# Kernel optimization log

Measured on AMD Instinct MI355X. Metric: run time of the kernel, lower is better.

Reference implementation:

```python
import jax, jax.numpy as jnp
import numpy as np

B, U1, U2 = 2, 3072, 3072
IF = 256      # in_feat_dim
FD = 256      # feat_dim
M = 4         # num_modes
D = IF // M   # attention_mode_dim = 64
STD = 0.02    # base_initializer_range
LN_EPS = 1e-12


def setup_inputs() -> dict:
    key = jax.random.key(0)
    ks = jax.random.split(key, 8)
    inp = {
        'query_feat': jax.random.normal(ks[0], (B, U1, IF), jnp.float32),
        'key_feat':   jax.random.normal(ks[1], (B, U2, IF), jnp.float32),
        # tied QK projection (key weight == query weight after tie_qk)
        'Wq':    jax.random.normal(ks[2], (M * D, IF), jnp.float32) * STD,
        # value projection of ExpandedFeatTrans.first_linear (v_has_bias=True)
        'Wv':    jax.random.normal(ks[3], (M * FD, IF), jnp.float32) * STD,
        'bv':    jnp.zeros((M * FD,), jnp.float32),
        # MMSharedMid shared linear
        'W_mid': jax.random.normal(ks[4], (FD, FD), jnp.float32) * STD,
        'b_mid': jnp.zeros((FD,), jnp.float32),
        # MMSharedOutput shared linear + LayerNorm
        'W_out': jax.random.normal(ks[5], (FD, FD), jnp.float32) * STD,
        'b_out': jnp.zeros((FD,), jnp.float32),
        'ln_g':  jnp.ones((FD,), jnp.float32),
        'ln_b':  jnp.zeros((FD,), jnp.float32),
        # LearnedSoftAggregate feat2score linear (FD -> 1)
        'W_agg': jax.random.normal(ks[6], (1, FD), jnp.float32) * STD,
        'b_agg': jnp.zeros((1,), jnp.float32),
    }
    return inp


def _layer_norm(x, g, b):
    mu = x.mean(-1, keepdims=True)
    var = ((x - mu) ** 2).mean(-1, keepdims=True)
    return (x - mu) * jax.lax.rsqrt(var + LN_EPS) * g + b


def reference(query_feat, key_feat, Wq, Wv, bv, W_mid, b_mid, W_out, b_out,
              ln_g, ln_b, W_agg, b_agg):
    # --- multi-mode cross attention with tied QK ---
    q = (query_feat @ Wq.T).reshape(B, U1, M, D).transpose(0, 2, 1, 3)  # b m u d
    k = (key_feat   @ Wq.T).reshape(B, U2, M, D).transpose(0, 2, 1, 3)  # b m v d
    scores = jnp.einsum('bmud,bmvd->bmuv', q, k) / np.float32(np.sqrt(D))
    probs = jax.nn.softmax(scores, axis=-1)                              # b m u v

    # --- ExpandedFeatTrans: per-mode value projection + fusion ---
    v = (key_feat @ Wv.T + bv).reshape(B, U2, M, FD).transpose(0, 2, 1, 3)  # b m v f
    fused = jnp.einsum('bmuv,bmvf->bmuf', probs, v)                          # b m u f

    # --- MMSharedMid FFN (shared linear + exact gelu; dropout=0) ---
    mid = jax.nn.gelu(fused @ W_mid.T + b_mid, approximate=False)

    # --- MMSharedOutput: shared linear + residual + LayerNorm ---
    outp = _layer_norm(mid @ W_out.T + b_out + fused, ln_g, ln_b)            # b m u f

    # --- LearnedSoftAggregate over modes (group_dim=1) ---
    mode_scores = (outp @ W_agg.T + b_agg)[..., 0]                           # b m u
    agg_probs = jax.nn.softmax(mode_scores, axis=1)
    trans_feat = (outp * agg_probs[..., None]).sum(axis=1)                   # b u f
    return trans_feat
```

## Files before the change

kernel.cpp:

```cpp
#include <hip/hip_runtime.h>
#include <hip/hip_bf16.h>
#include <cstdint>
#include <cstddef>

typedef __attribute__((ext_vector_type(8))) short     bf16x8;
typedef __attribute__((ext_vector_type(4))) float     f32x4;
typedef __attribute__((ext_vector_type(4))) unsigned short u16x4;

using as1_void = __attribute__((address_space(1))) void;
using as3_void = __attribute__((address_space(3))) void;

#define MFMA16(a,b,c) __builtin_amdgcn_mfma_f32_16x16x32_bf16((a),(b),(c),0,0,0)

__device__ __forceinline__ unsigned short f2bf(float f) {
  union { float f; unsigned u; } v; v.f = f;
  unsigned r = v.u + 0x7fffu + ((v.u >> 16) & 1u);
  return (unsigned short)(r >> 16);
}
__device__ __forceinline__ float bf2f(unsigned short h) {
  union { unsigned u; float f; } v; v.u = ((unsigned)h) << 16; return v.f;
}
__device__ __forceinline__ unsigned cvt_pk_bf16(float lo, float hi) {
  unsigned r;
  asm volatile("v_cvt_pk_bf16_f32 %0, %1, %2" : "=v"(r) : "v"(lo), "v"(hi));
  return r;
}

__device__ __forceinline__ void gload16(const void* g, void* l) {
  __builtin_amdgcn_global_load_lds((const as1_void*)g, (as3_void*)l, 16, 0, 0);
}

constexpr size_t oXq  = 0;
constexpr size_t oXk  = oXq + 1572864ull * 2;
constexpr size_t oWq  = oXk + 1572864ull * 2;
constexpr size_t oWv  = oWq + 65536ull   * 2;
constexpr size_t oWm  = oWv + 262144ull  * 2;
constexpr size_t oWo  = oWm + 65536ull   * 2;
constexpr size_t oQb  = oWo + 65536ull   * 2;
constexpr size_t oKb  = oQb + 1572864ull * 2;
constexpr size_t oVb  = oKb + 1572864ull * 2;
constexpr size_t oPa  = oVb + 6291456ull * 2;
constexpr size_t oMl  = oPa + 12582912ull * 2;

__global__ __launch_bounds__(256) void cvt_kernel(
    const float* __restrict__ q, const float* __restrict__ k,
    const float* __restrict__ wq, const float* __restrict__ wv,
    const float* __restrict__ wm, const float* __restrict__ wo,
    unsigned short* __restrict__ ws) {
  int i4 = (blockIdx.x * 256 + threadIdx.x) * 4;
  const float* src; int local;
  if (i4 < 1572864)       { src = q;  local = i4; }
  else if (i4 < 3145728)  { src = k;  local = i4 - 1572864; }
  else if (i4 < 3211264)  { src = wq; local = i4 - 3145728; }
  else if (i4 < 3473408)  { src = wv; local = i4 - 3211264; }
  else if (i4 < 3538944)  { src = wm; local = i4 - 3473408; }
  else                    { src = wo; local = i4 - 3538944; }
  f32x4 v = *(const f32x4*)(src + local);
  u16x4 o;
  o.x = f2bf(v.x); o.y = f2bf(v.y); o.z = f2bf(v.z); o.w = f2bf(v.w);
  *(u16x4*)(ws + i4) = o;
}

__global__ __launch_bounds__(256) void proj_kernel(const float* __restrict__ bv,
                                                   char* __restrict__ wsb) {
  int lane = threadIdx.x & 63, wid = threadIdx.x >> 6;
  int rowblk = blockIdx.x % 384;
  int ny = blockIdx.x / 384;
  int r0 = rowblk * 16;

  const unsigned short* X = (const unsigned short*)(wsb + (ny == 0 ? oXq : oXk));
  const unsigned short* W;
  if (ny <= 1) W = (const unsigned short*)(wsb + oWq);
  else         W = (const unsigned short*)(wsb + oWv) + (size_t)(ny - 2) * 256 * 256;

  int arow = r0 + (lane & 15);
  const unsigned short* Xp = X + (size_t)arow * 256 + ((lane >> 4) * 8);
  int n0 = wid * 64;

  f32x4 acc[4];
#pragma unroll
  for (int bt = 0; bt < 4; ++bt) acc[bt] = (f32x4){0.f, 0.f, 0.f, 0.f};

#pragma unroll
  for (int ks = 0; ks < 8; ++ks) {
    bf16x8 af = *(const bf16x8*)(Xp + ks * 32);
#pragma unroll
    for (int bt = 0; bt < 4; ++bt) {
      int n = n0 + bt * 16 + (lane & 15);
      bf16x8 bf = *(const bf16x8*)(W + (size_t)n * 256 + ks * 32 + ((lane >> 4) * 8));
      acc[bt] = MFMA16(af, bf, acc[bt]);
    }
  }

  int b = r0 / 3072, u0 = r0 % 3072;
  int ubase = u0 + ((lane >> 4) * 4);

  if (ny <= 1) {
    unsigned short* outp = (unsigned short*)(wsb + (ny == 0 ? oQb : oKb));
    float scale = (ny == 0) ? 0.125f : 1.0f;
    int m = wid;
#pragma unroll
    for (int bt = 0; bt < 4; ++bt) {
      int d = bt * 16 + (lane & 15);
#pragma unroll
      for (int r = 0; r < 4; ++r) {
        outp[((size_t)(b * 4 + m) * 3072 + (ubase + r)) * 64 + d] = f2bf(acc[bt][r] * scale);
      }
    }
  } else {
    unsigned short* vbT = (unsigned short*)(wsb + oVb);
    int mchunk = ny - 2;
#pragma unroll
    for (int bt = 0; bt < 4; ++bt) {
      int f = n0 + bt * 16 + (lane & 15);
      float bias = bv[mchunk * 256 + f];
      u16x4 pk;
#pragma unroll
      for (int r = 0; r < 4; ++r) pk[r] = f2bf(acc[bt][r] + bias);
      *(u16x4*)(vbT + ((size_t)(b * 4 + mchunk) * 256 + f) * 3072 + ubase) = pk;
    }
  }
}

__global__ __launch_bounds__(256, 3) void attn_kernel(char* __restrict__ wsb) {
  __shared__ unsigned short sK[64 * 64];
  __shared__ unsigned short sV[256 * 64];
  __shared__ unsigned short sP[4][16 * 64];
  __shared__ float sCr[4];
  __shared__ float sInv[4][16];

  const int lane = threadIdx.x & 63, wid = threadIdx.x >> 6;
  const int lq = lane & 15, hi = lane >> 4;
  const int lr3 = lane >> 3, lc3 = lane & 7;
  const int fh = wid >> 1, gp = wid & 1;
  const int bm = blockIdx.x & 7;
  const int z = blockIdx.x >> 3;
  const int qt = z >> 1, kvh = z & 1;
  const int q0 = qt * 64;
  const int kvbase = kvh * 1536;
  const int key = lq & 7;

  const unsigned short* qb = (const unsigned short*)(wsb + oQb) + (size_t)bm * 3072 * 64;
  const unsigned short* kb = (const unsigned short*)(wsb + oKb) + (size_t)bm * 3072 * 64;
  const unsigned short* vb = (const unsigned short*)(wsb + oVb) + (size_t)bm * 256 * 3072;

  const unsigned short* qp = qb + (size_t)(q0 + wid * 16 + lq) * 64 + hi * 8;
  const bf16x8 qf0 = *(const bf16x8*)(qp);
  const bf16x8 qf1 = *(const bf16x8*)(qp + 32);
  asm volatile("s_waitcnt vmcnt(0)" ::: "memory");

  const unsigned short* pk[2];
  unsigned short* dk[2];
#pragma unroll
  for (int i = 0; i < 2; ++i) {
    int ch = wid * 2 + i;
    int r = ch * 8 + lr3;
    int cs = lc3 ^ (r & 7);
    pk[i] = kb + (size_t)(kvbase + r) * 64 + cs * 8;
    dk[i] = &sK[ch * 512];
  }
  const unsigned short* pv[8];
  unsigned short* dv[8];
#pragma unroll
  for (int i = 0; i < 8; ++i) {
    int ch = i * 4 + wid;
    int f = ch * 8 + lr3;
    int cs = lc3 ^ (f & 7);
    pv[i] = vb + (size_t)f * 3072 + kvbase + cs * 8;
    dv[i] = &sV[ch * 512];
  }

  f32x4 acc[2][8];
#pragma unroll
  for (int g = 0; g < 2; ++g)
#pragma unroll
    for (int ft = 0; ft < 8; ++ft) acc[g][ft] = (f32x4){0.f, 0.f, 0.f, 0.f};
  float mrun = -1e30f, lrun = 0.f;

  char* myP = (char*)&sP[wid][0];
  const int g0 = gp * 2, g1 = gp * 2 + 1;
  char* rP0 = (char*)&sP[g0][0];
  char* rP1 = (char*)&sP[g1][0];

  gload16(pk[0], dk[0]); gload16(pk[1], dk[1]);
  pk[0] += 4096; pk[1] += 4096;

  for (int kt = 0; kt < 24; ++kt) {
#pragma unroll
    for (int i = 0; i < 8; ++i) { gload16(pv[i], dv[i]); pv[i] += 64; }

    asm volatile("s_waitcnt vmcnt(8)" ::: "memory");
    __builtin_amdgcn_sched_barrier(0);
    __builtin_amdgcn_s_barrier();

    bf16x8 kc0[4], kc1[4];
#pragma unroll
    for (int t = 0; t < 4; ++t) {
      const unsigned short* kr = &sK[(t * 16 + lq) * 64];
      kc0[t] = *(const bf16x8*)(kr + ((hi ^ key) * 8));
      kc1[t] = *(const bf16x8*)(kr + (((hi + 4) ^ key) * 8));
    }
    f32x4 s[4];
#pragma unroll
    for (int t = 0; t < 4; ++t) {
      f32x4 zz = (f32x4){0.f, 0.f, 0.f, 0.f};
      zz = MFMA16(kc0[t], qf0, zz);
      zz = MFMA16(kc1[t], qf1, zz);
      s[t] = zz;
    }

    float pmax = s[0][0];
#pragma unroll
    for (int t = 0; t < 4; ++t)
#pragma unroll
      for (int r = 0; r < 4; ++r) pmax = fmaxf(pmax, s[t][r]);
    pmax = fmaxf(pmax, __shfl_xor(pmax, 16));
    pmax = fmaxf(pmax, __shfl_xor(pmax, 32));

    float cr = 1.0f;
    if (__any(pmax > mrun + 8.0f)) {
      float mnew = fmaxf(mrun, pmax);
      cr = __builtin_amdgcn_exp2f((mrun - mnew) * 1.44269504f);
      lrun *= cr; mrun = mnew;
    }
    if (lane == 0) sCr[wid] = cr;

    const float mk = mrun * 1.44269504f;
    float ps[4][4];
    float psum = 0.f;
#pragma unroll
    for (int t = 0; t < 4; ++t)
#pragma unroll
      for (int r = 0; r < 4; ++r) {
        float p = __builtin_amdgcn_exp2f(s[t][r] * 1.44269504f - mk);
        ps[t][r] = p; psum += p;
      }
    psum += __shfl_xor(psum, 16);
    psum += __shfl_xor(psum, 32);
    lrun += psum;

#pragma unroll
    for (int t = 0; t < 4; ++t) {
      unsigned w0 = cvt_pk_bf16(ps[t][0], ps[t][1]);
      unsigned w1 = cvt_pk_bf16(ps[t][2], ps[t][3]);
      int c = (2 * t + (hi >> 1)) ^ key;
      *(uint2*)(myP + lq * 128 + (c << 4) + ((hi & 1) << 3)) = make_uint2(w0, w1);
    }

    asm volatile("s_waitcnt vmcnt(0) lgkmcnt(0)" ::: "memory");
    __builtin_amdgcn_sched_barrier(0);
    __builtin_amdgcn_s_barrier();

    if (kt < 23) {
      gload16(pk[0], dk[0]); gload16(pk[1], dk[1]);
      pk[0] += 4096; pk[1] += 4096;
    }

    float c0 = sCr[g0], c1 = sCr[g1];
    if (c0 != 1.0f) {
#pragma unroll
      for (int ft = 0; ft < 8; ++ft) {
        acc[0][ft][0] *= c0; acc[0][ft][1] *= c0;
        acc[0][ft][2] *= c0; acc[0][ft][3] *= c0;
      }
    }
    if (c1 != 1.0f) {
#pragma unroll
      for (int ft = 0; ft < 8; ++ft) {
        acc[1][ft][0] *= c1; acc[1][ft][1] *= c1;
        acc[1][ft][2] *= c1; acc[1][ft][3] *= c1;
      }
    }

    bf16x8 pb00 = *(const bf16x8*)(rP0 + lq * 128 + ((hi ^ key) << 4));
    bf16x8 pb01 = *(const bf16x8*)(rP0 + lq * 128 + (((4 + hi) ^ key) << 4));
    bf16x8 pb10 = *(const bf16x8*)(rP1 + lq * 128 + ((hi ^ key) << 4));
    bf16x8 pb11 = *(const bf16x8*)(rP1 + lq * 128 + (((4 + hi) ^ key) << 4));

    __builtin_amdgcn_s_setprio(1);
#pragma unroll
    for (int ft = 0; ft < 8; ++ft) {
      const unsigned short* vr = &sV[(fh * 128 + ft * 16 + lq) * 64];
      bf16x8 vf0 = *(const bf16x8*)(vr + ((hi ^ key) * 8));
      bf16x8 vf1 = *(const bf16x8*)(vr + (((4 + hi) ^ key) * 8));
      acc[0][ft] = MFMA16(vf0, pb00, acc[0][ft]);
      acc[0][ft] = MFMA16(vf1, pb01, acc[0][ft]);
      acc[1][ft] = MFMA16(vf0, pb10, acc[1][ft]);
      acc[1][ft] = MFMA16(vf1, pb11, acc[1][ft]);
    }
    __builtin_amdgcn_s_setprio(0);

    asm volatile("s_waitcnt lgkmcnt(0)" ::: "memory");
    __builtin_amdgcn_sched_barrier(0);
    __builtin_amdgcn_s_barrier();
  }

  if (hi == 0) {
    sInv[wid][lq] = 1.0f / lrun;
    float* ml = (float*)(wsb + oMl);
    size_t qi = (size_t)(kvh * 8 + bm) * 3072 + q0 + wid * 16 + lq;
    *(float2*)(ml + qi * 2) = make_float2(mrun, lrun);
  }
  __syncthreads();

  unsigned short* paB = (unsigned short*)(wsb + oPa) + (size_t)(kvh * 8 + bm) * 3072 * 256;
#pragma unroll
  for (int gi = 0; gi < 2; ++gi) {
    int g = gp * 2 + gi;
    float inv = sInv[g][lq];
    unsigned short* orow = paB + (size_t)(q0 + g * 16 + lq) * 256 + fh * 128 + hi * 4;
#pragma unroll
    for (int ft = 0; ft < 8; ++ft) {
      u16x4 pk4;
#pragma unroll
      for (int r = 0; r < 4; ++r) pk4[r] = f2bf(acc[gi][ft][r] * inv);
      *(u16x4*)(orow + ft * 16) = pk4;
    }
  }
}

__global__ __launch_bounds__(256, 2) void ffn_kernel(char* __restrict__ wsb,
                                                     const float* __restrict__ bmid,
                                                     const float* __restrict__ bout,
                                                     const float* __restrict__ lng,
                                                     const float* __restrict__ lnb,
                                                     const float* __restrict__ wagg,
                                                     const float* __restrict__ bagg,
                                                     float* __restrict__ out) {
  __shared__ unsigned short sA[64 * 256];
  __shared__ unsigned short sM[64 * 256];
  __shared__ float redS[4][64], redQ[4][64], redC[4][64];
  __shared__ float sSc[64];
  __shared__ float sW0[64], sW1[64];

  const int lane = threadIdx.x & 63, wid = threadIdx.x >> 6;
  const int lq = lane & 15, hi = lane >> 4;
  const int b = blockIdx.x / 192;
  const int u0 = (blockIdx.x % 192) * 16;

  const unsigned short* Wm = (const unsigned short*)(wsb + oWm);
  const unsigned short* Wo = (const unsigned short*)(wsb + oWo);
  const unsigned short* pa = (const unsigned short*)(wsb + oPa);
  const float* mlb = (const float*)(wsb + oMl);

  if (threadIdx.x < 64) {
    int m = threadIdx.x >> 4, du = threadIdx.x & 15;
    size_t qi = (size_t)(b * 4 + m) * 3072 + u0 + du;
    float2 ml0 = *(const float2*)(mlb + qi * 2);
    float2 ml1 = *(const float2*)(mlb + (qi + 8ull * 3072) * 2);
    float M = fmaxf(ml0.x, ml1.x);
    float e0 = ml0.y * __builtin_amdgcn_exp2f((ml0.x - M) * 1.44269504f);
    float e1 = ml1.y * __builtin_amdgcn_exp2f((ml1.x - M) * 1.44269504f);
    float inv = 1.0f / (e0 + e1);
    sW0[threadIdx.x] = e0 * inv;
    sW1[threadIdx.x] = e1 * inv;
  }
  __syncthreads();

  {
    int t = threadIdx.x;
#pragma unroll
    for (int j = 0; j < 8; ++j) {
      int i = j * 256 + t;
      int row = i >> 5, c = i & 31;
      int m = row >> 4, du = row & 15;
      const unsigned short* p0 = pa + ((size_t)(b * 4 + m) * 3072 + u0 + du) * 256 + c * 8;
      bf16x8 a = *(const bf16x8*)(p0);
      bf16x8 bb = *(const bf16x8*)(p0 + 8ull * 3072 * 256);
      float w0 = sW0[row], w1 = sW1[row];
      u16x4 oA, oB;
#pragma unroll
      for (int e = 0; e < 4; ++e) {
        oA[e] = f2bf(w0 * bf2f((unsigned short)a[e]) + w1 * bf2f((unsigned short)bb[e]));
        oB[e] = f2bf(w0 * bf2f((unsigned short)a[e + 4]) + w1 * bf2f((unsigned short)bb[e + 4]));
      }
      unsigned short* dst = &sA[row * 256 + ((c ^ (row & 7)) << 3)];
      *(u16x4*)(dst) = oA;
      *(u16x4*)(dst + 4) = oB;
    }
  }
  __syncthreads();

  const int n0 = wid * 64;
  const int rowb = hi * 4;

  f32x4 acc1[4][4];
#pragma unroll
  for (int rg = 0; rg < 4; ++rg)
#pragma unroll
    for (int bt = 0; bt < 4; ++bt) acc1[rg][bt] = (f32x4){0.f, 0.f, 0.f, 0.f};
#pragma unroll
  for (int ks = 0; ks < 8; ++ks) {
    bf16x8 a[4];
#pragma unroll
    for (int rg = 0; rg < 4; ++rg)
      a[rg] = *(const bf16x8*)&sA[(rg * 16 + lq) * 256 + (((ks * 4 + hi) ^ (lq & 7)) << 3)];
#pragma unroll
    for (int bt = 0; bt < 4; ++bt) {
      int n = n0 + bt * 16 + lq;
      bf16x8 bfr = *(const bf16x8*)(Wm + (size_t)n * 256 + ks * 32 + hi * 8);
#pragma unroll
      for (int rg = 0; rg < 4; ++rg) acc1[rg][bt] = MFMA16(a[rg], bfr, acc1[rg][bt]);
    }
  }
#pragma unroll
  for (int bt = 0; bt < 4; ++bt) {
    int n = n0 + bt * 16 + lq;
    float bb = bmid[n];
#pragma unroll
    for (int rg = 0; rg < 4; ++rg)
#pragma unroll
      for (int r = 0; r < 4; ++r) {
        float x = acc1[rg][bt][r] + bb;
        float g = 0.5f * x * (1.0f + erff(x * 0.7071067811865475f));
        int row = rg * 16 + rowb + r;
        sM[row * 256 + (((n >> 3) ^ (row & 7)) << 3) + (n & 7)] = f2bf(g);
      }
  }
  __syncthreads();

  f32x4 acc2[4][4];
#pragma unroll
  for (int rg = 0; rg < 4; ++rg)
#pragma unroll
    for (int bt = 0; bt < 4; ++bt) acc2[rg][bt] = (f32x4){0.f, 0.f, 0.f, 0.f};
#pragma unroll
  for (int ks = 0; ks < 8; ++ks) {
    bf16x8 a[4];
#pragma unroll
    for (int rg = 0; rg < 4; ++rg)
      a[rg] = *(const bf16x8*)&sM[(rg * 16 + lq) * 256 + (((ks * 4 + hi) ^ (lq & 7)) << 3)];
#pragma unroll
    for (int bt = 0; bt < 4; ++bt) {
      int n = n0 + bt * 16 + lq;
      bf16x8 bfr = *(const bf16x8*)(Wo + (size_t)n * 256 + ks * 32 + hi * 8);
#pragma unroll
      for (int rg = 0; rg < 4; ++rg) acc2[rg][bt] = MFMA16(a[rg], bfr, acc2[rg][bt]);
    }
  }

  float sS[4][4], sQ[4][4];
#pragma unroll
  for (int rg = 0; rg < 4; ++rg)
#pragma unroll
    for (int r = 0; r < 4; ++r) { sS[rg][r] = 0.f; sQ[rg][r] = 0.f; }
#pragma unroll
  for (int bt = 0; bt < 4; ++bt) {
    int n = n0 + bt * 16 + lq;
    float bo = bout[n];
#pragma unroll
    for (int rg = 0; rg < 4; ++rg)
#pragma unroll
      for (int r = 0; r < 4; ++r) {
        int row = rg * 16 + rowb + r;
        float res = bf2f(sA[row * 256 + (((n >> 3) ^ (row & 7)) << 3) + (n & 7)]);
        float x = acc2[rg][bt][r] + bo + res;
        acc2[rg][bt][r] = x;
        sS[rg][r] += x;
        sQ[rg][r] += x * x;
      }
  }
#pragma unroll
  for (int rg = 0; rg < 4; ++rg)
#pragma unroll
    for (int r = 0; r < 4; ++r) {
#pragma unroll
      for (int off = 1; off < 16; off <<= 1) {
        sS[rg][r] += __shfl_xor(sS[rg][r], off);
        sQ[rg][r] += __shfl_xor(sQ[rg][r], off);
      }
    }
  if (lq == 0) {
#pragma unroll
    for (int rg = 0; rg < 4; ++rg)
#pragma unroll
      for (int r = 0; r < 4; ++r) {
        int row = rg * 16 + rowb + r;
        redS[wid][row] = sS[rg][r]; redQ[wid][row] = sQ[rg][r];
      }
  }
  __syncthreads();

  float scp[4][4];
#pragma unroll
  for (int rg = 0; rg < 4; ++rg)
#pragma unroll
    for (int r = 0; r < 4; ++r) {
      int row = rg * 16 + rowb + r;
      float ts = redS[0][row] + redS[1][row] + redS[2][row] + redS[3][row];
      float tq = redQ[0][row] + redQ[1][row] + redQ[2][row] + redQ[3][row];
      float mean = ts * (1.0f / 256.0f);
      float var = tq * (1.0f / 256.0f) - mean * mean;
      float rs = rsqrtf(var + 1e-12f);
      float sc = 0.f;
#pragma unroll
      for (int bt = 0; bt < 4; ++bt) {
        int n = n0 + bt * 16 + lq;
        float o = (acc2[rg][bt][r] - mean) * rs * lng[n] + lnb[n];
        acc2[rg][bt][r] = o;
        sc += o * wagg[n];
      }
      scp[rg][r] = sc;
    }
#pragma unroll
  for (int rg = 0; rg < 4; ++rg)
#pragma unroll
    for (int r = 0; r < 4; ++r) {
#pragma unroll
      for (int off = 1; off < 16; off <<= 1) scp[rg][r] += __shfl_xor(scp[rg][r], off);
    }
  if (lq == 0) {
#pragma unroll
    for (int rg = 0; rg < 4; ++rg)
#pragma unroll
      for (int r = 0; r < 4; ++r) redC[wid][rg * 16 + rowb + r] = scp[rg][r];
  }
  __syncthreads();

  if (threadIdx.x < 64) {
    int t = threadIdx.x;
    sSc[t] = redC[0][t] + redC[1][t] + redC[2][t] + redC[3][t] + bagg[0];
  }
  __syncthreads();

  float wmode[4][4];
#pragma unroll
  for (int r = 0; r < 4; ++r) {
    int du = rowb + r;
    float s0 = sSc[du], s1 = sSc[16 + du], s2 = sSc[32 + du], s3 = sSc[48 + du];
    float mx = fmaxf(fmaxf(s0, s1), fmaxf(s2, s3));
    float e0 = __builtin_amdgcn_exp2f((s0 - mx) * 1.44269504f);
    float e1 = __builtin_amdgcn_exp2f((s1 - mx) * 1.44269504f);
    float e2 = __builtin_amdgcn_exp2f((s2 - mx) * 1.44269504f);
    float e3 = __builtin_amdgcn_exp2f((s3 - mx) * 1.44269504f);
    float inv = 1.0f / (e0 + e1 + e2 + e3);
    wmode[r][0] = e0 * inv; wmode[r][1] = e1 * inv;
    wmode[r][2] = e2 * inv; wmode[r][3] = e3 * inv;
  }
#pragma unroll
  for (int bt = 0; bt < 4; ++bt) {
    int n = n0 + bt * 16 + lq;
#pragma unroll
    for (int r = 0; r < 4; ++r) {
      int du = rowb + r;
      float val = wmode[r][0] * acc2[0][bt][r] + wmode[r][1] * acc2[1][bt][r]
                + wmode[r][2] * acc2[2][bt][r] + wmode[r][3] * acc2[3][bt][r];
      out[((size_t)(b * 3072 + u0 + du)) * 256 + n] = val;
    }
  }
}

extern "C" void kernel_launch(void* const* d_in, const int* in_sizes, int n_in,
                              void* d_out, int out_size, void* d_ws, size_t ws_size,
                              hipStream_t stream) {
  const float* q  = (const float*)d_in[0];
  const float* k  = (const float*)d_in[1];
  const float* wq = (const float*)d_in[2];
  const float* wv = (const float*)d_in[3];
  const float* bv = (const float*)d_in[4];
  const float* wm = (const float*)d_in[5];
  const float* bm = (const float*)d_in[6];
  const float* wo = (const float*)d_in[7];
  const float* bo = (const float*)d_in[8];
  const float* lg = (const float*)d_in[9];
  const float* lb = (const float*)d_in[10];
  const float* wa = (const float*)d_in[11];
  const float* ba = (const float*)d_in[12];
  char* wsb = (char*)d_ws;

  cvt_kernel<<<3520, 256, 0, stream>>>(q, k, wq, wv, wm, wo, (unsigned short*)wsb);
  proj_kernel<<<2304, 256, 0, stream>>>(bv, wsb);
  attn_kernel<<<768, 256, 0, stream>>>(wsb);
  ffn_kernel<<<384, 256, 0, stream>>>(wsb, bm, bo, lg, lb, wa, ba, (float*)d_out);
}
```

Measured before the change: 151.8 us.

## Repartition attention PV work per wave and halve FFN tile with mode-interleaved rows

In the attention kernel each wave now owns a 64-wide feature slice across all four query groups, rather than 128 features across two groups. Every V fragment read from LDS is therefore reused by four MFMAs instead of two, and LDS addresses are precomputed outside the loop. The FFN kernel processes 8 tokens per block instead of 16, with the four modes interleaved inside each 16-row MFMA tile so the mode-softmax reduction happens within a lane's accumulator registers. This doubles the FFN grid and raises launch bounds to 3 blocks per SM for more parallelism, at the cost of reloading weight fragments from global memory in more blocks.

```diff
diff --git a/kernel.cpp b/kernel.cpp
--- a/kernel.cpp
+++ b/kernel.cpp
@@ -132,7 +132,6 @@
   const int lane = threadIdx.x & 63, wid = threadIdx.x >> 6;
   const int lq = lane & 15, hi = lane >> 4;
   const int lr3 = lane >> 3, lc3 = lane & 7;
-  const int fh = wid >> 1, gp = wid & 1;
   const int bm = blockIdx.x & 7;
   const int z = blockIdx.x >> 3;
   const int qt = z >> 1, kvh = z & 1;
@@ -170,17 +169,27 @@
     dv[i] = &sV[ch * 512];
   }
 
-  f32x4 acc[2][8];
-#pragma unroll
-  for (int g = 0; g < 2; ++g)
-#pragma unroll
-    for (int ft = 0; ft < 8; ++ft) acc[g][ft] = (f32x4){0.f, 0.f, 0.f, 0.f};
+  const int o0 = (hi ^ key) << 4;
+  const int o1 = ((hi + 4) ^ key) << 4;
+  const char* kB0 = (const char*)sK + lq * 128 + o0;
+  const char* kB1 = (const char*)sK + lq * 128 + o1;
+  const char* vB0 = (const char*)sV + (size_t)(wid * 64 + lq) * 128 + o0;
+  const char* vB1 = (const char*)sV + (size_t)(wid * 64 + lq) * 128 + o1;
+  char* myP = (char*)&sP[wid][0] + lq * 128;
+  int wofs[4];
+#pragma unroll
+  for (int t = 0; t < 4; ++t)
+    wofs[t] = ((((2 * t + (hi >> 1)) ^ key) << 4) + ((hi & 1) << 3));
+  const char* pB[4];
+#pragma unroll
+  for (int g = 0; g < 4; ++g) pB[g] = (const char*)&sP[g][0] + lq * 128;
+
+  f32x4 acc[4][4];
+#pragma unroll
+  for (int g = 0; g < 4; ++g)
+#pragma unroll
+    for (int ft = 0; ft < 4; ++ft) acc[g][ft] = (f32x4){0.f, 0.f, 0.f, 0.f};
   float mrun = -1e30f, lrun = 0.f;
-
-  char* myP = (char*)&sP[wid][0];
-  const int g0 = gp * 2, g1 = gp * 2 + 1;
-  char* rP0 = (char*)&sP[g0][0];
-  char* rP1 = (char*)&sP[g1][0];
 
   gload16(pk[0], dk[0]); gload16(pk[1], dk[1]);
   pk[0] += 4096; pk[1] += 4096;
@@ -196,9 +205,8 @@
     bf16x8 kc0[4], kc1[4];
 #pragma unroll
     for (int t = 0; t < 4; ++t) {
-      const unsigned short* kr = &sK[(t * 16 + lq) * 64];
-      kc0[t] = *(const bf16x8*)(kr + ((hi ^ key) * 8));
-      kc1[t] = *(const bf16x8*)(kr + (((hi + 4) ^ key) * 8));
+      kc0[t] = *(const bf16x8*)(kB0 + t * 2048);
+      kc1[t] = *(const bf16x8*)(kB1 + t * 2048);
     }
     f32x4 s[4];
 #pragma unroll
@@ -243,8 +251,7 @@
     for (int t = 0; t < 4; ++t) {
       unsigned w0 = cvt_pk_bf16(ps[t][0], ps[t][1]);
       unsigned w1 = cvt_pk_bf16(ps[t][2], ps[t][3]);
-      int c = (2 * t + (hi >> 1)) ^ key;
-      *(uint2*)(myP + lq * 128 + (c << 4) + ((hi & 1) << 3)) = make_uint2(w0, w1);
+      *(uint2*)(myP + wofs[t]) = make_uint2(w0, w1);
     }
 
     asm volatile("s_waitcnt vmcnt(0) lgkmcnt(0)" ::: "memory");
@@ -256,37 +263,37 @@
       pk[0] += 4096; pk[1] += 4096;
     }
 
-    float c0 = sCr[g0], c1 = sCr[g1];
-    if (c0 != 1.0f) {
-#pragma unroll
-      for (int ft = 0; ft < 8; ++ft) {
-        acc[0][ft][0] *= c0; acc[0][ft][1] *= c0;
-        acc[0][ft][2] *= c0; acc[0][ft][3] *= c0;
-      }
-    }
-    if (c1 != 1.0f) {
-#pragma unroll
-      for (int ft = 0; ft < 8; ++ft) {
-        acc[1][ft][0] *= c1; acc[1][ft][1] *= c1;
-        acc[1][ft][2] *= c1; acc[1][ft][3] *= c1;
-      }
-    }
-
-    bf16x8 pb00 = *(const bf16x8*)(rP0 + lq * 128 + ((hi ^ key) << 4));
-    bf16x8 pb01 = *(const bf16x8*)(rP0 + lq * 128 + (((4 + hi) ^ key) << 4));
-    bf16x8 pb10 = *(const bf16x8*)(rP1 + lq * 128 + ((hi ^ key) << 4));
-    bf16x8 pb11 = *(const bf16x8*)(rP1 + lq * 128 + (((4 + hi) ^ key) << 4));
+    float c[4];
+#pragma unroll
+    for (int g = 0; g < 4; ++g) c[g] = sCr[g];
+#pragma unroll
+    for (int g = 0; g < 4; ++g) {
+      if (c[g] != 1.0f) {
+#pragma unroll
+        for (int ft = 0; ft < 4; ++ft) {
+          acc[g][ft][0] *= c[g]; acc[g][ft][1] *= c[g];
+          acc[g][ft][2] *= c[g]; acc[g][ft][3] *= c[g];
+        }
+      }
+    }
+
+    bf16x8 pbs[4][2];
+#pragma unroll
+    for (int g = 0; g < 4; ++g) {
+      pbs[g][0] = *(const bf16x8*)(pB[g] + o0);
+      pbs[g][1] = *(const bf16x8*)(pB[g] + o1);
+    }
 
     __builtin_amdgcn_s_setprio(1);
 #pragma unroll
-    for (int ft = 0; ft < 8; ++ft) {
-      const unsigned short* vr = &sV[(fh * 128 + ft * 16 + lq) * 64];
-      bf16x8 vf0 = *(const bf16x8*)(vr + ((hi ^ key) * 8));
-      bf16x8 vf1 = *(const bf16x8*)(vr + (((4 + hi) ^ key) * 8));
-      acc[0][ft] = MFMA16(vf0, pb00, acc[0][ft]);
-      acc[0][ft] = MFMA16(vf1, pb01, acc[0][ft]);
-      acc[1][ft] = MFMA16(vf0, pb10, acc[1][ft]);
-      acc[1][ft] = MFMA16(vf1, pb11, acc[1][ft]);
+    for (int ft = 0; ft < 4; ++ft) {
+      bf16x8 vf0 = *(const bf16x8*)(vB0 + ft * 2048);
+      bf16x8 vf1 = *(const bf16x8*)(vB1 + ft * 2048);
+#pragma unroll
+      for (int g = 0; g < 4; ++g) {
+        acc[g][ft] = MFMA16(vf0, pbs[g][0], acc[g][ft]);
+        acc[g][ft] = MFMA16(vf1, pbs[g][1], acc[g][ft]);
+      }
     }
     __builtin_amdgcn_s_setprio(0);
 
@@ -305,21 +312,20 @@
 
   unsigned short* paB = (unsigned short*)(wsb + oPa) + (size_t)(kvh * 8 + bm) * 3072 * 256;
 #pragma unroll
-  for (int gi = 0; gi < 2; ++gi) {
-    int g = gp * 2 + gi;
+  for (int g = 0; g < 4; ++g) {
     float inv = sInv[g][lq];
-    unsigned short* orow = paB + (size_t)(q0 + g * 16 + lq) * 256 + fh * 128 + hi * 4;
-#pragma unroll
-    for (int ft = 0; ft < 8; ++ft) {
+    unsigned short* orow = paB + (size_t)(q0 + g * 16 + lq) * 256 + wid * 64 + hi * 4;
+#pragma unroll
+    for (int ft = 0; ft < 4; ++ft) {
       u16x4 pk4;
 #pragma unroll
-      for (int r = 0; r < 4; ++r) pk4[r] = f2bf(acc[gi][ft][r] * inv);
+      for (int r = 0; r < 4; ++r) pk4[r] = f2bf(acc[g][ft][r] * inv);
       *(u16x4*)(orow + ft * 16) = pk4;
     }
   }
 }
 
-__global__ __launch_bounds__(256, 2) void ffn_kernel(char* __restrict__ wsb,
+__global__ __launch_bounds__(256, 3) void ffn_kernel(char* __restrict__ wsb,
                                                      const float* __restrict__ bmid,
                                                      const float* __restrict__ bout,
                                                      const float* __restrict__ lng,
@@ -327,24 +333,24 @@
                                                      const float* __restrict__ wagg,
                                                      const float* __restrict__ bagg,
                                                      float* __restrict__ out) {
-  __shared__ unsigned short sA[64 * 256];
-  __shared__ unsigned short sM[64 * 256];
-  __shared__ float redS[4][64], redQ[4][64], redC[4][64];
-  __shared__ float sSc[64];
-  __shared__ float sW0[64], sW1[64];
+  __shared__ unsigned short sA[32 * 256];
+  __shared__ unsigned short sM[32 * 256];
+  __shared__ float redS[4][32], redQ[4][32], redC[4][32];
+  __shared__ float sSc[32];
+  __shared__ float sW0[32], sW1[32];
 
   const int lane = threadIdx.x & 63, wid = threadIdx.x >> 6;
   const int lq = lane & 15, hi = lane >> 4;
-  const int b = blockIdx.x / 192;
-  const int u0 = (blockIdx.x % 192) * 16;
+  const int b = blockIdx.x / 384;
+  const int u0 = (blockIdx.x % 384) * 8;
 
   const unsigned short* Wm = (const unsigned short*)(wsb + oWm);
   const unsigned short* Wo = (const unsigned short*)(wsb + oWo);
   const unsigned short* pa = (const unsigned short*)(wsb + oPa);
   const float* mlb = (const float*)(wsb + oMl);
 
-  if (threadIdx.x < 64) {
-    int m = threadIdx.x >> 4, du = threadIdx.x & 15;
+  if (threadIdx.x < 32) {
+    int m = threadIdx.x & 3, du = threadIdx.x >> 2;
     size_t qi = (size_t)(b * 4 + m) * 3072 + u0 + du;
     float2 ml0 = *(const float2*)(mlb + qi * 2);
     float2 ml1 = *(const float2*)(mlb + (qi + 8ull * 3072) * 2);
@@ -360,10 +366,10 @@
   {
     int t = threadIdx.x;
 #pragma unroll
-    for (int j = 0; j < 8; ++j) {
+    for (int j = 0; j < 4; ++j) {
       int i = j * 256 + t;
       int row = i >> 5, c = i & 31;
-      int m = row >> 4, du = row & 15;
+      int m = row & 3, du = row >> 2;
       const unsigned short* p0 = pa + ((size_t)(b * 4 + m) * 3072 + u0 + du) * 256 + c * 8;
       bf16x8 a = *(const bf16x8*)(p0);
       bf16x8 bb = *(const bf16x8*)(p0 + 8ull * 3072 * 256);
@@ -384,23 +390,23 @@
   const int n0 = wid * 64;
   const int rowb = hi * 4;
 
-  f32x4 acc1[4][4];
-#pragma unroll
-  for (int rg = 0; rg < 4; ++rg)
+  f32x4 acc1[2][4];
+#pragma unroll
+  for (int rg = 0; rg < 2; ++rg)
 #pragma unroll
     for (int bt = 0; bt < 4; ++bt) acc1[rg][bt] = (f32x4){0.f, 0.f, 0.f, 0.f};
 #pragma unroll
   for (int ks = 0; ks < 8; ++ks) {
-    bf16x8 a[4];
-#pragma unroll
-    for (int rg = 0; rg < 4; ++rg)
+    bf16x8 a[2];
+#pragma unroll
+    for (int rg = 0; rg < 2; ++rg)
       a[rg] = *(const bf16x8*)&sA[(rg * 16 + lq) * 256 + (((ks * 4 + hi) ^ (lq & 7)) << 3)];
 #pragma unroll
     for (int bt = 0; bt < 4; ++bt) {
       int n = n0 + bt * 16 + lq;
       bf16x8 bfr = *(const bf16x8*)(Wm + (size_t)n * 256 + ks * 32 + hi * 8);
 #pragma unroll
-      for (int rg = 0; rg < 4; ++rg) acc1[rg][bt] = MFMA16(a[rg], bfr, acc1[rg][bt]);
+      for (int rg = 0; rg < 2; ++rg) acc1[rg][bt] = MFMA16(a[rg], bfr, acc1[rg][bt]);
     }
   }
 #pragma unroll
@@ -408,7 +414,7 @@
     int n = n0 + bt * 16 + lq;
     float bb = bmid[n];
 #pragma unroll
-    for (int rg = 0; rg < 4; ++rg)
+    for (int rg = 0; rg < 2; ++rg)
 #pragma unroll
       for (int r = 0; r < 4; ++r) {
         float x = acc1[rg][bt][r] + bb;
@@ -419,29 +425,29 @@
   }
   __syncthreads();
 
-  f32x4 acc2[4][4];
-#pragma unroll
-  for (int rg = 0; rg < 4; ++rg)
+  f32x4 acc2[2][4];
+#pragma unroll
+  for (int rg = 0; rg < 2; ++rg)
 #pragma unroll
     for (int bt = 0; bt < 4; ++bt) acc2[rg][bt] = (f32x4){0.f, 0.f, 0.f, 0.f};
 #pragma unroll
   for (int ks = 0; ks < 8; ++ks) {
-    bf16x8 a[4];
-#pragma unroll
-    for (int rg = 0; rg < 4; ++rg)
+    bf16x8 a[2];
+#pragma unroll
+    for (int rg = 0; rg < 2; ++rg)
       a[rg] = *(const bf16x8*)&sM[(rg * 16 + lq) * 256 + (((ks * 4 + hi) ^ (lq & 7)) << 3)];
 #pragma unroll
     for (int bt = 0; bt < 4; ++bt) {
       int n = n0 + bt * 16 + lq;
       bf16x8 bfr = *(const bf16x8*)(Wo + (size_t)n * 256 + ks * 32 + hi * 8);
 #pragma unroll
-      for (int rg = 0; rg < 4; ++rg) acc2[rg][bt] = MFMA16(a[rg], bfr, acc2[rg][bt]);
-    }
-  }
-
-  float sS[4][4], sQ[4][4];
-#pragma unroll
-  for (int rg = 0; rg < 4; ++rg)
+      for (int rg = 0; rg < 2; ++rg) acc2[rg][bt] = MFMA16(a[rg], bfr, acc2[rg][bt]);
+    }
+  }
+
+  float sS[2][4], sQ[2][4];
+#pragma unroll
+  for (int rg = 0; rg < 2; ++rg)
 #pragma unroll
     for (int r = 0; r < 4; ++r) { sS[rg][r] = 0.f; sQ[rg][r] = 0.f; }
 #pragma unroll
@@ -449,7 +455,7 @@
     int n = n0 + bt * 16 + lq;
     float bo = bout[n];
 #pragma unroll
-    for (int rg = 0; rg < 4; ++rg)
+    for (int rg = 0; rg < 2; ++rg)
 #pragma unroll
       for (int r = 0; r < 4; ++r) {
         int row = rg * 16 + rowb + r;
@@ -461,7 +467,7 @@
       }
   }
 #pragma unroll
-  for (int rg = 0; rg < 4; ++rg)
+  for (int rg = 0; rg < 2; ++rg)
 #pragma unroll
     for (int r = 0; r < 4; ++r) {
 #pragma unroll
@@ -472,7 +478,7 @@
     }
   if (lq == 0) {
 #pragma unroll
-    for (int rg = 0; rg < 4; ++rg)
+    for (int rg = 0; rg < 2; ++rg)
 #pragma unroll
       for (int r = 0; r < 4; ++r) {
         int row = rg * 16 + rowb + r;
@@ -481,9 +487,9 @@
   }
   __syncthreads();
 
-  float scp[4][4];
-#pragma unroll
-  for (int rg = 0; rg < 4; ++rg)
+  float scp[2][4];
+#pragma unroll
+  for (int rg = 0; rg < 2; ++rg)
 #pragma unroll
     for (int r = 0; r < 4; ++r) {
       int row = rg * 16 + rowb + r;
@@ -503,7 +509,7 @@
       scp[rg][r] = sc;
     }
 #pragma unroll
-  for (int rg = 0; rg < 4; ++rg)
+  for (int rg = 0; rg < 2; ++rg)
 #pragma unroll
     for (int r = 0; r < 4; ++r) {
 #pragma unroll
@@ -511,40 +517,41 @@
     }
   if (lq == 0) {
 #pragma unroll
-    for (int rg = 0; rg < 4; ++rg)
+    for (int rg = 0; rg < 2; ++rg)
 #pragma unroll
       for (int r = 0; r < 4; ++r) redC[wid][rg * 16 + rowb + r] = scp[rg][r];
   }
   __syncthreads();
 
-  if (threadIdx.x < 64) {
+  if (threadIdx.x < 32) {
     int t = threadIdx.x;
     sSc[t] = redC[0][t] + redC[1][t] + redC[2][t] + redC[3][t] + bagg[0];
   }
   __syncthreads();
 
-  float wmode[4][4];
-#pragma unroll
-  for (int r = 0; r < 4; ++r) {
-    int du = rowb + r;
-    float s0 = sSc[du], s1 = sSc[16 + du], s2 = sSc[32 + du], s3 = sSc[48 + du];
+  float wm[2][4];
+#pragma unroll
+  for (int rg = 0; rg < 2; ++rg) {
+    int du = rg * 4 + hi;
+    float s0 = sSc[du * 4 + 0], s1 = sSc[du * 4 + 1];
+    float s2 = sSc[du * 4 + 2], s3 = sSc[du * 4 + 3];
     float mx = fmaxf(fmaxf(s0, s1), fmaxf(s2, s3));
     float e0 = __builtin_amdgcn_exp2f((s0 - mx) * 1.44269504f);
     float e1 = __builtin_amdgcn_exp2f((s1 - mx) * 1.44269504f);
     float e2 = __builtin_amdgcn_exp2f((s2 - mx) * 1.44269504f);
     float e3 = __builtin_amdgcn_exp2f((s3 - mx) * 1.44269504f);
     float inv = 1.0f / (e0 + e1 + e2 + e3);
-    wmode[r][0] = e0 * inv; wmode[r][1] = e1 * inv;
-    wmode[r][2] = e2 * inv; wmode[r][3] = e3 * inv;
+    wm[rg][0] = e0 * inv; wm[rg][1] = e1 * inv;
+    wm[rg][2] = e2 * inv; wm[rg][3] = e3 * inv;
   }
 #pragma unroll
   for (int bt = 0; bt < 4; ++bt) {
     int n = n0 + bt * 16 + lq;
 #pragma unroll
-    for (int r = 0; r < 4; ++r) {
-      int du = rowb + r;
-      float val = wmode[r][0] * acc2[0][bt][r] + wmode[r][1] * acc2[1][bt][r]
-                + wmode[r][2] * acc2[2][bt][r] + wmode[r][3] * acc2[3][bt][r];
+    for (int rg = 0; rg < 2; ++rg) {
+      int du = rg * 4 + hi;
+      float val = wm[rg][0] * acc2[rg][bt][0] + wm[rg][1] * acc2[rg][bt][1]
+                + wm[rg][2] * acc2[rg][bt][2] + wm[rg][3] * acc2[rg][bt][3];
       out[((size_t)(b * 3072 + u0 + du)) * 256 + n] = val;
     }
   }
@@ -571,5 +578,5 @@
   cvt_kernel<<<3520, 256, 0, stream>>>(q, k, wq, wv, wm, wo, (unsigned short*)wsb);
   proj_kernel<<<2304, 256, 0, stream>>>(bv, wsb);
   attn_kernel<<<768, 256, 0, stream>>>(wsb);
-  ffn_kernel<<<384, 256, 0, stream>>>(wsb, bm, bo, lg, lb, wa, ba, (float*)d_out);
-}
+  ffn_kernel<<<768, 256, 0, stream>>>(wsb, bm, bo, lg, lb, wa, ba, (float*)d_out);
+}
```

Measured after the change: 160.7 us. 5.8% more time.
